# Performance work log

Measured on AMD Instinct MI355X. Metric: run time of the kernel, lower is better.

## Reference

```python
import jax, jax.numpy as jnp
import numpy as np

B, N, D, H = 8, 1024, 768, 12
HD = D // H
SCALE = HD ** -0.5

def setup_inputs() -> dict:
    key = jax.random.key(0)
    k1, k2, k3, k4 = jax.random.split(key, 4)
    x = jax.random.normal(k1, (B, N, D), dtype=jnp.float32)
    weight = jax.random.uniform(k2, (B, N), dtype=jnp.float32)
    W_qkv = jax.random.normal(k3, (D, 3 * D), dtype=jnp.float32) * (D ** -0.5)
    W_msa = jax.random.normal(k4, (D, D), dtype=jnp.float32) * (D ** -0.5)
    b_msa = jnp.zeros((D,), dtype=jnp.float32)
    return {"x": x, "weight": weight, "W_qkv": W_qkv, "W_msa": W_msa, "b_msa": b_msa}

def reference(x, weight, W_qkv, W_msa, b_msa):
    # QKV projection (no bias), then elementwise per-token gate
    qkv = jnp.einsum('bnd,de->bne', x, W_qkv)          # [B,N,3D]
    qkv = weight[:, :, None] * qkv
    qkv = qkv.reshape(B, N, 3, H, HD).transpose(2, 0, 3, 1, 4)  # [3,B,H,N,hd]
    q, k, v = qkv[0], qkv[1], qkv[2]
    A = jnp.einsum('bhnd,bhmd->bhnm', q, k) * SCALE    # [B,H,N,N]
    A = jax.nn.softmax(A, axis=-1)
    out = jnp.einsum('bhnm,bhmd->bhnd', A, v)          # [B,H,N,hd]
    out = out.transpose(0, 2, 1, 3).reshape(B, N, D)
    return jnp.einsum('bnd,de->bne', out, W_msa) + b_msa
```

## Files before the change

### kernel.cpp

```cpp
#include <hip/hip_runtime.h>
#include <hip/hip_bf16.h>


typedef __attribute__((ext_vector_type(8))) short bf8;
typedef __attribute__((ext_vector_type(4))) float f4;

#define QSCALE 0.1803368801111204f
#define MFMA16 __builtin_amdgcn_mfma_f32_16x16x32_bf16

static __device__ __forceinline__ short bf16_of(float f) {
    union { float f; unsigned u; } a; a.f = f;
    unsigned r = a.u + 0x7FFFu + ((a.u >> 16) & 1u);
    return (short)(r >> 16);
}

static __device__ __forceinline__ unsigned bfpk(float lo, float hi) {
    float2 t; t.x = lo; t.y = hi;
    __hip_bfloat162 b = __float22bfloat162_rn(t);
    union { __hip_bfloat162 b; unsigned u; } c; c.b = b;
    return c.u;
}

static __device__ __forceinline__ void async16(const short* g, short* l) {
    __builtin_amdgcn_global_load_lds(
        (const __attribute__((address_space(1))) void*)g,
        (__attribute__((address_space(3))) void*)l, 16, 0, 0);
}

static __device__ __forceinline__ void transpose64(
        const float* __restrict__ w, short* __restrict__ wt,
        int K, int E, int k0, int e0, int tid, short (*t)[65]) {
#pragma unroll
    for (int p = 0; p < 16; ++p) {
        int idx = p * 256 + tid;
        int r = idx >> 6, c = idx & 63;
        t[r][c] = bf16_of(w[(k0 + r) * E + e0 + c]);
    }
    __syncthreads();
#pragma unroll
    for (int p = 0; p < 16; ++p) {
        int idx = p * 256 + tid;
        int r = idx >> 6, c = idx & 63;
        wt[(e0 + r) * K + k0 + c] = t[c][r];
    }
}

__global__ __launch_bounds__(256) void k_prep(
        const float* __restrict__ x, const float* __restrict__ gate,
        short* __restrict__ xb,
        const float* __restrict__ Wqkv, short* __restrict__ wtq,
        const float* __restrict__ Wmsa, short* __restrict__ wtm) {
    __shared__ short t[64][65];
    const int bid = blockIdx.x, tid = threadIdx.x;
    if (bid < 3072) {
        int i = bid * 256 + tid;
        const float g = gate[i / 96];
        const f4* sp = (const f4*)x;
        f4 a = sp[2 * i], b = sp[2 * i + 1];
        union { bf8 v; short h[8]; } o;
        o.h[0] = bf16_of(a[0] * g); o.h[1] = bf16_of(a[1] * g);
        o.h[2] = bf16_of(a[2] * g); o.h[3] = bf16_of(a[3] * g);
        o.h[4] = bf16_of(b[0] * g); o.h[5] = bf16_of(b[1] * g);
        o.h[6] = bf16_of(b[2] * g); o.h[7] = bf16_of(b[7 - 4] * g);
        o.h[6] = bf16_of(b[2] * g); o.h[7] = bf16_of(b[3] * g);
        ((bf8*)xb)[i] = o.v;
    } else if (bid < 3504) {
        int tt = bid - 3072;
        transpose64(Wqkv, wtq, 768, 2304, (tt / 36) * 64, (tt % 36) * 64, tid, t);
    } else {
        int tt = bid - 3504;
        transpose64(Wmsa, wtm, 768, 768, (tt / 12) * 64, (tt % 12) * 64, tid, t);
    }
}

__global__ __launch_bounds__(256, 2) void k_gemm_qkv(
        const short* __restrict__ xb, const short* __restrict__ wtq,
        short* __restrict__ qb, short* __restrict__ kb, short* __restrict__ vt) {
    __shared__ short lds[34816];
    const int tid = threadIdx.x, lane = tid & 63;
    const int l16 = lane & 15, quad = lane >> 4;
    const int wm = tid >> 6;

    const int wg = blockIdx.x;
    const int swz = (wg & 7) * 128 + (wg >> 3);
    const int mI = swz >> 4, nI = swz & 15;
    const int m0 = mI * 128, n0 = nI * 144;

    const short* gA = xb + m0 * 768;
    const short* gB = wtq + n0 * 768;

    auto stage = [&](int buf, int k0) {
        short* base = lds + buf * 8704;
#pragma unroll
        for (int j = 0; j < 2; ++j) {
            int p = j * 256 + tid, row = p >> 2;
            int gc = (p & 3) ^ ((row >> 1) & 3);
            async16(gA + row * 768 + k0 + gc * 8, base + p * 8);
        }
#pragma unroll
        for (int j = 0; j < 2; ++j) {
            int p = j * 256 + tid, row = p >> 2;
            int gc = (p & 3) ^ ((row >> 1) & 3);
            async16(gB + row * 768 + k0 + gc * 8, base + 4096 + p * 8);
        }
        if (tid < 64) {
            int p = 512 + tid, row = p >> 2;
            int gc = (p & 3) ^ ((row >> 1) & 3);
            async16(gB + row * 768 + k0 + gc * 8, base + 4096 + p * 8);
        }
    };

    auto rdA = [&](const short* base, int mf) {
        int row = wm * 32 + mf * 16 + l16;
        return *(const bf8*)(base + row * 32 +
                             ((quad ^ ((row >> 1) & 3)) << 3));
    };
    auto rdB = [&](const short* base, int nf) {
        int row = nf * 16 + l16;
        return *(const bf8*)(base + 4096 + row * 32 +
                             ((quad ^ ((row >> 1) & 3)) << 3));
    };

    f4 z = {0.f, 0.f, 0.f, 0.f};
    f4 acc[2][9];
#pragma unroll
    for (int mf = 0; mf < 2; ++mf)
#pragma unroll
        for (int nf = 0; nf < 9; ++nf) acc[mf][nf] = z;

    stage(0, 0); stage(1, 32); stage(2, 64);
    if (wm == 0) asm volatile("s_waitcnt vmcnt(10)" ::: "memory");
    else         asm volatile("s_waitcnt vmcnt(8)" ::: "memory");
    __builtin_amdgcn_s_barrier();

#pragma unroll 4
    for (int t = 0; t < 24; ++t) {
        const short* cur = lds + (t & 3) * 8704;
        bf8 af0 = rdA(cur, 0);
        bf8 af1 = rdA(cur, 1);
        bf8 bfr[9];
#pragma unroll
        for (int nf = 0; nf < 9; ++nf) bfr[nf] = rdB(cur, nf);
        if (t < 21) stage((t + 3) & 3, (t + 3) * 32);
        __builtin_amdgcn_s_setprio(1);
#pragma unroll
        for (int nf = 0; nf < 9; ++nf) {
            acc[0][nf] = MFMA16(af0, bfr[nf], acc[0][nf], 0, 0, 0);
            acc[1][nf] = MFMA16(af1, bfr[nf], acc[1][nf], 0, 0, 0);
        }
        __builtin_amdgcn_s_setprio(0);
        if (t < 21) {
            if (wm == 0) asm volatile("s_waitcnt vmcnt(10)" ::: "memory");
            else         asm volatile("s_waitcnt vmcnt(8)" ::: "memory");
        } else if (t == 21) {
            if (wm == 0) asm volatile("s_waitcnt vmcnt(5)" ::: "memory");
            else         asm volatile("s_waitcnt vmcnt(4)" ::: "memory");
        } else if (t == 22) {
            asm volatile("s_waitcnt vmcnt(0)" ::: "memory");
        }
        if (t < 23) __builtin_amdgcn_s_barrier();
    }

    const int bI = m0 >> 10, nn0 = m0 & 1023;
#pragma unroll
    for (int nf = 0; nf < 9; ++nf) {
        const int ct = n0 + nf * 16;
        if (ct < 1536) {
            const int which = (ct >= 768) ? 1 : 0;
            const int h = (ct - which * 768) >> 6;
            const int hd = (ct & 63) + l16;
            short* dst = (which ? kb : qb) + (bI * 12 + h) * 65536 + hd;
#pragma unroll
            for (int mf = 0; mf < 2; ++mf)
#pragma unroll
                for (int r = 0; r < 4; ++r) {
                    const int nn = nn0 + wm * 32 + mf * 16 + quad * 4 + r;
                    const float val = acc[mf][nf][r];
                    dst[nn * 64] = bf16_of(which ? val : val * QSCALE);
                }
        }
    }
    const int vlo = (n0 >= 1536) ? n0 : 1536;
    const int vcnt = n0 + 144 - vlo;
    const int npass = (vcnt > 0) ? vcnt / 48 : 0;
    for (int p = 0; p < npass; ++p) {
        __syncthreads();
        const int c0 = vlo + p * 48;
#pragma unroll
        for (int nf = 0; nf < 9; ++nf) {
            const int ct = n0 + nf * 16;
            if (ct >= c0 && ct < c0 + 48) {
                const int lcol = ct - c0 + l16;
#pragma unroll
                for (int mf = 0; mf < 2; ++mf)
#pragma unroll
                    for (int r = 0; r < 4; ++r) {
                        const int row = wm * 32 + mf * 16 + quad * 4 + r;
                        lds[lcol * 136 + row] = bf16_of(acc[mf][nf][r]);
                    }
            }
        }
        __syncthreads();
        const int vg0 = c0 - 1536;
#pragma unroll
        for (int u = 0; u < 3; ++u) {
            const int idx = u * 256 + tid;
            const int lc = idx >> 4, ck = idx & 15;
            const int vg = vg0 + lc;
            const int h = vg >> 6, hd = vg & 63;
            bf8 vv = *(const bf8*)(lds + lc * 136 + ck * 8);
            *(bf8*)(vt + ((bI * 12 + h) * 64 + hd) * 1024 + nn0 + ck * 8) = vv;
        }
    }
}

__global__ __launch_bounds__(256, 2) void k_gemm_final(
        const short* __restrict__ attn, const short* __restrict__ wtm,
        const float* __restrict__ bias, float* __restrict__ out) {
    __shared__ short lds[28672];
    const int tid = threadIdx.x, lane = tid & 63;
    const int l16 = lane & 15, quad = lane >> 4, rx = l16 & 7;
    const int wm = tid >> 6;

    const int wg = blockIdx.x;
    const int swz = (wg & 7) * 64 + (wg >> 3);
    const int mI = swz >> 3, nI = swz & 7;
    const int m0 = mI * 128, n0 = nI * 96;

    const short* gA = attn + m0 * 768;
    const short* gB = wtm + n0 * 768;

    auto stageA = [&](int buf, int k0) {
        short* base = lds + buf * 14336;
#pragma unroll
        for (int j = 0; j < 4; ++j) {
            int p = j * 256 + tid, row = p >> 3;
            int gc = (p & 7) ^ (row & 7);
            async16(gA + row * 768 + k0 + gc * 8, base + p * 8);
        }
    };
    auto stageB = [&](int buf, int k0) {
        short* base = lds + buf * 14336 + 8192;
#pragma unroll
        for (int j = 0; j < 3; ++j) {
            int p = j * 256 + tid, row = p >> 3;
            int gc = (p & 7) ^ (row & 7);
            async16(gB + row * 768 + k0 + gc * 8, base + p * 8);
        }
    };
    auto rdA = [&](const short* base, int mf, int ks) {
        return *(const bf8*)(base + (wm * 32 + mf * 16 + l16) * 64 +
                             (((ks * 4 + quad) ^ rx) << 3));
    };
    auto rdB = [&](const short* base, int nf, int ks) {
        return *(const bf8*)(base + 8192 + (nf * 16 + l16) * 64 +
                             (((ks * 4 + quad) ^ rx) << 3));
    };

    f4 z = {0.f, 0.f, 0.f, 0.f};
    f4 acc[2][6];
#pragma unroll
    for (int mf = 0; mf < 2; ++mf)
#pragma unroll
        for (int nf = 0; nf < 6; ++nf) acc[mf][nf] = z;

    stageA(0, 0); stageB(0, 0);
    asm volatile("s_waitcnt vmcnt(0)" ::: "memory");
    __builtin_amdgcn_s_barrier();

#pragma unroll 2
    for (int t = 0; t < 12; ++t) {
        const short* cur = lds + (t & 1) * 14336;
        bf8 af[2][2];
        af[0][0] = rdA(cur, 0, 0); af[0][1] = rdA(cur, 0, 1);
        af[1][0] = rdA(cur, 1, 0); af[1][1] = rdA(cur, 1, 1);
        bf8 bfr[3][2];
#pragma unroll
        for (int nf = 0; nf < 3; ++nf) { bfr[nf][0] = rdB(cur, nf, 0); bfr[nf][1] = rdB(cur, nf, 1); }
        if (t < 11) stageA((t + 1) & 1, (t + 1) * 64);
        __builtin_amdgcn_s_setprio(1);
#pragma unroll
        for (int mf = 0; mf < 2; ++mf)
#pragma unroll
            for (int nf = 0; nf < 3; ++nf) {
                acc[mf][nf] = MFMA16(af[mf][0], bfr[nf][0], acc[mf][nf], 0, 0, 0);
                acc[mf][nf] = MFMA16(af[mf][1], bfr[nf][1], acc[mf][nf], 0, 0, 0);
            }
        __builtin_amdgcn_s_setprio(0);
        bf8 bfh[3][2];
#pragma unroll
        for (int nf = 0; nf < 3; ++nf) { bfh[nf][0] = rdB(cur, nf + 3, 0); bfh[nf][1] = rdB(cur, nf + 3, 1); }
        if (t < 11) stageB((t + 1) & 1, (t + 1) * 64);
        __builtin_amdgcn_s_setprio(1);
#pragma unroll
        for (int mf = 0; mf < 2; ++mf)
#pragma unroll
            for (int nf = 0; nf < 3; ++nf) {
                acc[mf][nf + 3] = MFMA16(af[mf][0], bfh[nf][0], acc[mf][nf + 3], 0, 0, 0);
                acc[mf][nf + 3] = MFMA16(af[mf][1], bfh[nf][1], acc[mf][nf + 3], 0, 0, 0);
            }
        __builtin_amdgcn_s_setprio(0);
        asm volatile("s_waitcnt vmcnt(0)" ::: "memory");
        __builtin_amdgcn_s_barrier();
    }

#pragma unroll
    for (int nf = 0; nf < 6; ++nf) {
        const int e = n0 + nf * 16 + l16;
        const float bv = bias[e];
#pragma unroll
        for (int mf = 0; mf < 2; ++mf)
#pragma unroll
            for (int r = 0; r < 4; ++r) {
                const int row = m0 + wm * 32 + mf * 16 + quad * 4 + r;
                out[row * 768 + e] = acc[mf][nf][r] + bv;
            }
    }
}

__global__ __launch_bounds__(256, 3) void k_attn(const short* __restrict__ qb,
                                                 const short* __restrict__ kb,
                                                 const short* __restrict__ vt,
                                                 short* __restrict__ attn) {
    __shared__ short Ks[2][4096];
    __shared__ short Vs[2][4096];
    const int tid = threadIdx.x, wave = tid >> 6, lane = tid & 63;
    const int l16 = lane & 15, quad = lane >> 4;
    const int bh = blockIdx.x;
    const int b = bh / 12, h = bh - b * 12;
    const int m_base = blockIdx.y * 128 + wave * 32;
    const short* qh = qb + bh * 65536;
    const short* kh = kb + bh * 65536;
    const short* vh = vt + bh * 65536;

    const int rA = ((l16 >> 2) << 3) + (l16 & 3);
    const int fK = (((rA >> 3) & 1) << 2) + (rA & 3);
    const int sK = (quad ^ fK) * 8;
    const int oAlo = rA * 64 + sK;
    const int oAhi = rA * 64 + (sK ^ 32);
    const int oBlo = oAlo + 256, oBhi = oAhi + 256;
    const int fV = (((l16 >> 3) & 1) << 2) + (l16 & 3);
    const int oV = l16 * 64 + ((quad ^ fV) * 8);

    const short* qp0 = qh + (m_base + l16) * 64 + quad * 8;
    bf8 qf00 = *(const bf8*)(qp0);
    bf8 qf01 = *(const bf8*)(qp0 + 32);
    const short* qp1 = qp0 + 16 * 64;
    bf8 qf10 = *(const bf8*)(qp1);
    bf8 qf11 = *(const bf8*)(qp1 + 32);

    union { bf8 v; short h[8]; } onef;
#pragma unroll
    for (int i = 0; i < 8; ++i) onef.h[i] = (short)0x3F80;

    f4 z = {0.f, 0.f, 0.f, 0.f};
    f4 acc0[4] = {z, z, z, z};
    f4 acc1[4] = {z, z, z, z};
    f4 accl0 = z, accl1 = z;

    auto stage = [&](int buf, int j0) {
#pragma unroll
        for (int j = 0; j < 2; ++j) {
            int idx = j * 256 + tid;
            int row = idx >> 3;
            int fr = (((row >> 3) & 1) << 2) + (row & 3);
            int gc = (idx & 7) ^ fr;
            async16(kh + (j0 + row) * 64 + gc * 8, Ks[buf] + idx * 8);
            async16(vh + row * 1024 + j0 + gc * 8, Vs[buf] + idx * 8);
        }
    };

    stage(0, 0);
    int cur = 0;
    for (int it = 0; it < 16; ++it) {
        __builtin_amdgcn_s_waitcnt(0);
        __syncthreads();
        if (it + 1 < 16) stage(cur ^ 1, (it + 1) * 64);
        const short* Kc = Ks[cur];
        const short* Vc = Vs[cur];

#pragma unroll
        for (int jj = 0; jj < 64; jj += 32) {
            const short* kjj = Kc + jj * 64;
            bf8 kAlo = *(const bf8*)(kjj + oAlo);
            bf8 kAhi = *(const bf8*)(kjj + oAhi);
            bf8 kBlo = *(const bf8*)(kjj + oBlo);
            bf8 kBhi = *(const bf8*)(kjj + oBhi);
            bf8 vf0 = *(const bf8*)(Vc + 0 * 1024 + (oV ^ (jj ? 32 : 0)));
            bf8 vf1 = *(const bf8*)(Vc + 1 * 1024 + (oV ^ (jj ? 32 : 0)));
            bf8 vf2 = *(const bf8*)(Vc + 2 * 1024 + (oV ^ (jj ? 32 : 0)));
            bf8 vf3 = *(const bf8*)(Vc + 3 * 1024 + (oV ^ (jj ? 32 : 0)));

            {
                f4 sA = z, sB = z;
                __builtin_amdgcn_s_setprio(1);
                sA = MFMA16(kAlo, qf00, sA, 0, 0, 0);
                sA = MFMA16(kAhi, qf01, sA, 0, 0, 0);
                sB = MFMA16(kBlo, qf00, sB, 0, 0, 0);
                sB = MFMA16(kBhi, qf01, sB, 0, 0, 0);
                __builtin_amdgcn_s_setprio(0);
                float a0 = __builtin_amdgcn_exp2f(sA[0]);
                float a1 = __builtin_amdgcn_exp2f(sA[1]);
                float a2 = __builtin_amdgcn_exp2f(sA[2]);
                float a3 = __builtin_amdgcn_exp2f(sA[3]);
                float b0 = __builtin_amdgcn_exp2f(sB[0]);
                float b1 = __builtin_amdgcn_exp2f(sB[1]);
                float b2 = __builtin_amdgcn_exp2f(sB[2]);
                float b3 = __builtin_amdgcn_exp2f(sB[3]);
                union { bf8 v; unsigned u[4]; } p;
                p.u[0] = bfpk(a0, a1); p.u[1] = bfpk(a2, a3);
                p.u[2] = bfpk(b0, b1); p.u[3] = bfpk(b2, b3);
                __builtin_amdgcn_s_setprio(1);
                accl0 = MFMA16(onef.v, p.v, accl0, 0, 0, 0);
                acc0[0] = MFMA16(vf0, p.v, acc0[0], 0, 0, 0);
                acc0[1] = MFMA16(vf1, p.v, acc0[1], 0, 0, 0);
                acc0[2] = MFMA16(vf2, p.v, acc0[2], 0, 0, 0);
                acc0[3] = MFMA16(vf3, p.v, acc0[3], 0, 0, 0);
                __builtin_amdgcn_s_setprio(0);
            }
            {
                f4 sA = z, sB = z;
                __builtin_amdgcn_s_setprio(1);
                sA = MFMA16(kAlo, qf10, sA, 0, 0, 0);
                sA = MFMA16(kAhi, qf11, sA, 0, 0, 0);
                sB = MFMA16(kBlo, qf10, sB, 0, 0, 0);
                sB = MFMA16(kBhi, qf11, sB, 0, 0, 0);
                __builtin_amdgcn_s_setprio(0);
                float a0 = __builtin_amdgcn_exp2f(sA[0]);
                float a1 = __builtin_amdgcn_exp2f(sA[1]);
                float a2 = __builtin_amdgcn_exp2f(sA[2]);
                float a3 = __builtin_amdgcn_exp2f(sA[3]);
                float b0 = __builtin_amdgcn_exp2f(sB[0]);
                float b1 = __builtin_amdgcn_exp2f(sB[1]);
                float b2 = __builtin_amdgcn_exp2f(sB[2]);
                float b3 = __builtin_amdgcn_exp2f(sB[3]);
                union { bf8 v; unsigned u[4]; } p;
                p.u[0] = bfpk(a0, a1); p.u[1] = bfpk(a2, a3);
                p.u[2] = bfpk(b0, b1); p.u[3] = bfpk(b2, b3);
                __builtin_amdgcn_s_setprio(1);
                accl1 = MFMA16(onef.v, p.v, accl1, 0, 0, 0);
                acc1[0] = MFMA16(vf0, p.v, acc1[0], 0, 0, 0);
                acc1[1] = MFMA16(vf1, p.v, acc1[1], 0, 0, 0);
                acc1[2] = MFMA16(vf2, p.v, acc1[2], 0, 0, 0);
                acc1[3] = MFMA16(vf3, p.v, acc1[3], 0, 0, 0);
                __builtin_amdgcn_s_setprio(0);
            }
        }
        cur ^= 1;
    }

    const float inv0 = 1.f / accl0[0];
    const float inv1 = 1.f / accl1[0];
    const int row0 = (b << 10) + m_base + l16;
    short* op0 = attn + row0 * 768 + h * 64 + quad * 4;
    short* op1 = op0 + 16 * 768;
#pragma unroll
    for (int dt = 0; dt < 4; ++dt)
#pragma unroll
        for (int r = 0; r < 4; ++r) {
            op0[dt * 16 + r] = bf16_of(acc0[dt][r] * inv0);
            op1[dt * 16 + r] = bf16_of(acc1[dt][r] * inv1);
        }
}

extern "C" void kernel_launch(void* const* d_in, const int* in_sizes, int n_in,
                              void* d_out, int out_size, void* d_ws, size_t ws_size,
                              hipStream_t stream) {
    const float* x    = (const float*)d_in[0];
    const float* gate = (const float*)d_in[1];
    const float* Wqkv = (const float*)d_in[2];
    const float* Wmsa = (const float*)d_in[3];
    const float* bmsa = (const float*)d_in[4];
    float* out = (float*)d_out;

    char* ws = (char*)d_ws;
    short* xb  = (short*)(ws);
    short* wtq = (short*)(ws + 12582912);
    short* wtm = (short*)(ws + 16121856);
    short* qb  = (short*)(ws + 17301504);
    short* kb  = (short*)(ws + 29884416);
    short* vt  = (short*)(ws + 42467328);
    short* attn = xb;

    k_prep<<<3648, 256, 0, stream>>>(x, gate, xb, Wqkv, wtq, Wmsa, wtm);
    k_gemm_qkv<<<1024, 256, 0, stream>>>(xb, wtq, qb, kb, vt);
    k_attn<<<dim3(96, 8), 256, 0, stream>>>(qb, kb, vt, attn);
    k_gemm_final<<<512, 256, 0, stream>>>(attn, wtm, bmsa, out);
}
```

Baseline: 172.0 us.

## Enlarge QKV GEMM tile to 128x288 with 2x2 wave grid and triple buffering

The QKV projection GEMM now uses 128x288 output tiles per workgroup, split across a 2x2 wave layout with each wave computing 64x144. The grid halves to 512 workgroups, and the LDS pipeline goes from four stages to three to fit the larger tiles. The aim is more MFMA work per LDS fragment load and less redundant A-tile loading from global memory. The cost is many more accumulator registers (36 f4 per wave), fewer workgroups in the grid, and a shallower prefetch depth.

```diff
diff --git a/kernel.cpp b/kernel.cpp
--- a/kernel.cpp
+++ b/kernel.cpp
@@ -61,7 +61,6 @@
         o.h[0] = bf16_of(a[0] * g); o.h[1] = bf16_of(a[1] * g);
         o.h[2] = bf16_of(a[2] * g); o.h[3] = bf16_of(a[3] * g);
         o.h[4] = bf16_of(b[0] * g); o.h[5] = bf16_of(b[1] * g);
-        o.h[6] = bf16_of(b[2] * g); o.h[7] = bf16_of(b[7 - 4] * g);
         o.h[6] = bf16_of(b[2] * g); o.h[7] = bf16_of(b[3] * g);
         ((bf8*)xb)[i] = o.v;
     } else if (bid < 3504) {
@@ -76,21 +75,21 @@
 __global__ __launch_bounds__(256, 2) void k_gemm_qkv(
         const short* __restrict__ xb, const short* __restrict__ wtq,
         short* __restrict__ qb, short* __restrict__ kb, short* __restrict__ vt) {
-    __shared__ short lds[34816];
+    __shared__ short lds[39936];
     const int tid = threadIdx.x, lane = tid & 63;
     const int l16 = lane & 15, quad = lane >> 4;
-    const int wm = tid >> 6;
+    const int wv = tid >> 6, wm = wv >> 1, wn = wv & 1;
 
     const int wg = blockIdx.x;
-    const int swz = (wg & 7) * 128 + (wg >> 3);
-    const int mI = swz >> 4, nI = swz & 15;
-    const int m0 = mI * 128, n0 = nI * 144;
+    const int swz = (wg & 7) * 64 + (wg >> 3);
+    const int mI = swz >> 3, nI = swz & 7;
+    const int m0 = mI * 128, n0 = nI * 288;
 
     const short* gA = xb + m0 * 768;
     const short* gB = wtq + n0 * 768;
 
     auto stage = [&](int buf, int k0) {
-        short* base = lds + buf * 8704;
+        short* base = lds + buf * 13312;
 #pragma unroll
         for (int j = 0; j < 2; ++j) {
             int p = j * 256 + tid, row = p >> 2;
@@ -98,63 +97,61 @@
             async16(gA + row * 768 + k0 + gc * 8, base + p * 8);
         }
 #pragma unroll
-        for (int j = 0; j < 2; ++j) {
+        for (int j = 0; j < 4; ++j) {
             int p = j * 256 + tid, row = p >> 2;
             int gc = (p & 3) ^ ((row >> 1) & 3);
             async16(gB + row * 768 + k0 + gc * 8, base + 4096 + p * 8);
         }
-        if (tid < 64) {
-            int p = 512 + tid, row = p >> 2;
+        if (tid < 128) {
+            int p = 1024 + tid, row = p >> 2;
             int gc = (p & 3) ^ ((row >> 1) & 3);
             async16(gB + row * 768 + k0 + gc * 8, base + 4096 + p * 8);
         }
     };
 
     auto rdA = [&](const short* base, int mf) {
-        int row = wm * 32 + mf * 16 + l16;
+        int row = wm * 64 + mf * 16 + l16;
         return *(const bf8*)(base + row * 32 +
                              ((quad ^ ((row >> 1) & 3)) << 3));
     };
     auto rdB = [&](const short* base, int nf) {
-        int row = nf * 16 + l16;
+        int row = wn * 144 + nf * 16 + l16;
         return *(const bf8*)(base + 4096 + row * 32 +
                              ((quad ^ ((row >> 1) & 3)) << 3));
     };
 
     f4 z = {0.f, 0.f, 0.f, 0.f};
-    f4 acc[2][9];
-#pragma unroll
-    for (int mf = 0; mf < 2; ++mf)
+    f4 acc[4][9];
+#pragma unroll
+    for (int mf = 0; mf < 4; ++mf)
 #pragma unroll
         for (int nf = 0; nf < 9; ++nf) acc[mf][nf] = z;
 
-    stage(0, 0); stage(1, 32); stage(2, 64);
-    if (wm == 0) asm volatile("s_waitcnt vmcnt(10)" ::: "memory");
-    else         asm volatile("s_waitcnt vmcnt(8)" ::: "memory");
+    stage(0, 0); stage(1, 32);
+    if (wv < 2) asm volatile("s_waitcnt vmcnt(7)" ::: "memory");
+    else        asm volatile("s_waitcnt vmcnt(6)" ::: "memory");
     __builtin_amdgcn_s_barrier();
 
-#pragma unroll 4
+#pragma unroll 3
     for (int t = 0; t < 24; ++t) {
-        const short* cur = lds + (t & 3) * 8704;
-        bf8 af0 = rdA(cur, 0);
-        bf8 af1 = rdA(cur, 1);
+        const short* cur = lds + (t % 3) * 13312;
+        bf8 af[4];
+#pragma unroll
+        for (int mf = 0; mf < 4; ++mf) af[mf] = rdA(cur, mf);
         bf8 bfr[9];
 #pragma unroll
         for (int nf = 0; nf < 9; ++nf) bfr[nf] = rdB(cur, nf);
-        if (t < 21) stage((t + 3) & 3, (t + 3) * 32);
+        if (t < 22) stage((t + 2) % 3, (t + 2) * 32);
         __builtin_amdgcn_s_setprio(1);
 #pragma unroll
-        for (int nf = 0; nf < 9; ++nf) {
-            acc[0][nf] = MFMA16(af0, bfr[nf], acc[0][nf], 0, 0, 0);
-            acc[1][nf] = MFMA16(af1, bfr[nf], acc[1][nf], 0, 0, 0);
-        }
+        for (int mf = 0; mf < 4; ++mf)
+#pragma unroll
+            for (int nf = 0; nf < 9; ++nf)
+                acc[mf][nf] = MFMA16(af[mf], bfr[nf], acc[mf][nf], 0, 0, 0);
         __builtin_amdgcn_s_setprio(0);
-        if (t < 21) {
-            if (wm == 0) asm volatile("s_waitcnt vmcnt(10)" ::: "memory");
-            else         asm volatile("s_waitcnt vmcnt(8)" ::: "memory");
-        } else if (t == 21) {
-            if (wm == 0) asm volatile("s_waitcnt vmcnt(5)" ::: "memory");
-            else         asm volatile("s_waitcnt vmcnt(4)" ::: "memory");
+        if (t < 22) {
+            if (wv < 2) asm volatile("s_waitcnt vmcnt(7)" ::: "memory");
+            else        asm volatile("s_waitcnt vmcnt(6)" ::: "memory");
         } else if (t == 22) {
             asm volatile("s_waitcnt vmcnt(0)" ::: "memory");
         }
@@ -164,46 +161,45 @@
     const int bI = m0 >> 10, nn0 = m0 & 1023;
 #pragma unroll
     for (int nf = 0; nf < 9; ++nf) {
-        const int ct = n0 + nf * 16;
+        const int ct = n0 + wn * 144 + nf * 16;
         if (ct < 1536) {
             const int which = (ct >= 768) ? 1 : 0;
             const int h = (ct - which * 768) >> 6;
             const int hd = (ct & 63) + l16;
             short* dst = (which ? kb : qb) + (bI * 12 + h) * 65536 + hd;
 #pragma unroll
-            for (int mf = 0; mf < 2; ++mf)
+            for (int mf = 0; mf < 4; ++mf)
 #pragma unroll
                 for (int r = 0; r < 4; ++r) {
-                    const int nn = nn0 + wm * 32 + mf * 16 + quad * 4 + r;
+                    const int nn = nn0 + wm * 64 + mf * 16 + quad * 4 + r;
                     const float val = acc[mf][nf][r];
                     dst[nn * 64] = bf16_of(which ? val : val * QSCALE);
                 }
         }
     }
-    const int vlo = (n0 >= 1536) ? n0 : 1536;
-    const int vcnt = n0 + 144 - vlo;
-    const int npass = (vcnt > 0) ? vcnt / 48 : 0;
+    const int vstart = (n0 >= 1536) ? n0 : 1536;
+    const int npass = (n0 + 288 > vstart) ? (n0 + 288 - vstart) / 96 : 0;
     for (int p = 0; p < npass; ++p) {
         __syncthreads();
-        const int c0 = vlo + p * 48;
+        const int c0 = vstart + p * 96;
 #pragma unroll
         for (int nf = 0; nf < 9; ++nf) {
-            const int ct = n0 + nf * 16;
-            if (ct >= c0 && ct < c0 + 48) {
-                const int lcol = ct - c0 + l16;
-#pragma unroll
-                for (int mf = 0; mf < 2; ++mf)
+            const int ct = n0 + wn * 144 + nf * 16;
+            if (ct >= c0 && ct < c0 + 96) {
+                const int lc = ct - c0 + l16;
+#pragma unroll
+                for (int mf = 0; mf < 4; ++mf)
 #pragma unroll
                     for (int r = 0; r < 4; ++r) {
-                        const int row = wm * 32 + mf * 16 + quad * 4 + r;
-                        lds[lcol * 136 + row] = bf16_of(acc[mf][nf][r]);
+                        const int row = wm * 64 + mf * 16 + quad * 4 + r;
+                        lds[lc * 136 + row] = bf16_of(acc[mf][nf][r]);
                     }
             }
         }
         __syncthreads();
         const int vg0 = c0 - 1536;
 #pragma unroll
-        for (int u = 0; u < 3; ++u) {
+        for (int u = 0; u < 6; ++u) {
             const int idx = u * 256 + tid;
             const int lc = idx >> 4, ck = idx & 15;
             const int vg = vg0 + lc;
@@ -483,7 +479,7 @@
     short* attn = xb;
 
     k_prep<<<3648, 256, 0, stream>>>(x, gate, xb, Wqkv, wtq, Wmsa, wtm);
-    k_gemm_qkv<<<1024, 256, 0, stream>>>(xb, wtq, qb, kb, vt);
+    k_gemm_qkv<<<512, 256, 0, stream>>>(xb, wtq, qb, kb, vt);
     k_attn<<<dim3(96, 8), 256, 0, stream>>>(qb, kb, vt, attn);
     k_gemm_final<<<512, 256, 0, stream>>>(attn, wtm, bmsa, out);
 }
```

Result: slower. 218.3 us (+26.9%).

## Deepen async LDS pipelines in final GEMM and attention kernels

Applied to the files above, without the earlier changes.

The output-projection GEMM now uses a K-step of 32 with a 4-stage ring of LDS buffers and prefetches three stages ahead. Partial vmcnt waits replace full drains, with different counts per thread group because only half the threads issue the extra B load. The attention kernel moves from double to triple buffering of K/V tiles with vmcnt(4) waits, so global loads stay in flight across iterations. A duplicated store line in the prep kernel is also removed. This adds LDS use and per-thread waitcnt bookkeeping that must exactly match the number of issued loads.

```diff
diff --git a/kernel.cpp b/kernel.cpp
--- a/kernel.cpp
+++ b/kernel.cpp
@@ -61,7 +61,6 @@
         o.h[0] = bf16_of(a[0] * g); o.h[1] = bf16_of(a[1] * g);
         o.h[2] = bf16_of(a[2] * g); o.h[3] = bf16_of(a[3] * g);
         o.h[4] = bf16_of(b[0] * g); o.h[5] = bf16_of(b[1] * g);
-        o.h[6] = bf16_of(b[2] * g); o.h[7] = bf16_of(b[7 - 4] * g);
         o.h[6] = bf16_of(b[2] * g); o.h[7] = bf16_of(b[3] * g);
         ((bf8*)xb)[i] = o.v;
     } else if (bid < 3504) {
@@ -219,7 +218,7 @@
         const float* __restrict__ bias, float* __restrict__ out) {
     __shared__ short lds[28672];
     const int tid = threadIdx.x, lane = tid & 63;
-    const int l16 = lane & 15, quad = lane >> 4, rx = l16 & 7;
+    const int l16 = lane & 15, quad = lane >> 4;
     const int wm = tid >> 6;
 
     const int wg = blockIdx.x;
@@ -230,31 +229,35 @@
     const short* gA = attn + m0 * 768;
     const short* gB = wtm + n0 * 768;
 
-    auto stageA = [&](int buf, int k0) {
-        short* base = lds + buf * 14336;
-#pragma unroll
-        for (int j = 0; j < 4; ++j) {
-            int p = j * 256 + tid, row = p >> 3;
-            int gc = (p & 7) ^ (row & 7);
+    auto stage = [&](int buf, int k0) {
+        short* base = lds + buf * 7168;
+#pragma unroll
+        for (int j = 0; j < 2; ++j) {
+            int p = j * 256 + tid, row = p >> 2;
+            int gc = (p & 3) ^ ((row >> 1) & 3);
             async16(gA + row * 768 + k0 + gc * 8, base + p * 8);
         }
-    };
-    auto stageB = [&](int buf, int k0) {
-        short* base = lds + buf * 14336 + 8192;
-#pragma unroll
-        for (int j = 0; j < 3; ++j) {
-            int p = j * 256 + tid, row = p >> 3;
-            int gc = (p & 7) ^ (row & 7);
-            async16(gB + row * 768 + k0 + gc * 8, base + p * 8);
-        }
-    };
-    auto rdA = [&](const short* base, int mf, int ks) {
-        return *(const bf8*)(base + (wm * 32 + mf * 16 + l16) * 64 +
-                             (((ks * 4 + quad) ^ rx) << 3));
-    };
-    auto rdB = [&](const short* base, int nf, int ks) {
-        return *(const bf8*)(base + 8192 + (nf * 16 + l16) * 64 +
-                             (((ks * 4 + quad) ^ rx) << 3));
+        {
+            int p = tid, row = p >> 2;
+            int gc = (p & 3) ^ ((row >> 1) & 3);
+            async16(gB + row * 768 + k0 + gc * 8, base + 4096 + p * 8);
+        }
+        if (tid < 128) {
+            int p = 256 + tid, row = p >> 2;
+            int gc = (p & 3) ^ ((row >> 1) & 3);
+            async16(gB + row * 768 + k0 + gc * 8, base + 4096 + p * 8);
+        }
+    };
+
+    auto rdA = [&](const short* base, int mf) {
+        int row = wm * 32 + mf * 16 + l16;
+        return *(const bf8*)(base + row * 32 +
+                             ((quad ^ ((row >> 1) & 3)) << 3));
+    };
+    auto rdB = [&](const short* base, int nf) {
+        int row = nf * 16 + l16;
+        return *(const bf8*)(base + 4096 + row * 32 +
+                             ((quad ^ ((row >> 1) & 3)) << 3));
     };
 
     f4 z = {0.f, 0.f, 0.f, 0.f};
@@ -264,44 +267,37 @@
 #pragma unroll
         for (int nf = 0; nf < 6; ++nf) acc[mf][nf] = z;
 
-    stageA(0, 0); stageB(0, 0);
-    asm volatile("s_waitcnt vmcnt(0)" ::: "memory");
+    stage(0, 0); stage(1, 32); stage(2, 64);
+    if (tid < 128) asm volatile("s_waitcnt vmcnt(8)" ::: "memory");
+    else           asm volatile("s_waitcnt vmcnt(6)" ::: "memory");
     __builtin_amdgcn_s_barrier();
 
-#pragma unroll 2
-    for (int t = 0; t < 12; ++t) {
-        const short* cur = lds + (t & 1) * 14336;
-        bf8 af[2][2];
-        af[0][0] = rdA(cur, 0, 0); af[0][1] = rdA(cur, 0, 1);
-        af[1][0] = rdA(cur, 1, 0); af[1][1] = rdA(cur, 1, 1);
-        bf8 bfr[3][2];
-#pragma unroll
-        for (int nf = 0; nf < 3; ++nf) { bfr[nf][0] = rdB(cur, nf, 0); bfr[nf][1] = rdB(cur, nf, 1); }
-        if (t < 11) stageA((t + 1) & 1, (t + 1) * 64);
+#pragma unroll 4
+    for (int t = 0; t < 24; ++t) {
+        const short* cur = lds + (t & 3) * 7168;
+        bf8 af0 = rdA(cur, 0);
+        bf8 af1 = rdA(cur, 1);
+        bf8 bfr[6];
+#pragma unroll
+        for (int nf = 0; nf < 6; ++nf) bfr[nf] = rdB(cur, nf);
+        if (t < 21) stage((t + 3) & 3, (t + 3) * 32);
         __builtin_amdgcn_s_setprio(1);
 #pragma unroll
-        for (int mf = 0; mf < 2; ++mf)
-#pragma unroll
-            for (int nf = 0; nf < 3; ++nf) {
-                acc[mf][nf] = MFMA16(af[mf][0], bfr[nf][0], acc[mf][nf], 0, 0, 0);
-                acc[mf][nf] = MFMA16(af[mf][1], bfr[nf][1], acc[mf][nf], 0, 0, 0);
-            }
+        for (int nf = 0; nf < 6; ++nf) {
+            acc[0][nf] = MFMA16(af0, bfr[nf], acc[0][nf], 0, 0, 0);
+            acc[1][nf] = MFMA16(af1, bfr[nf], acc[1][nf], 0, 0, 0);
+        }
         __builtin_amdgcn_s_setprio(0);
-        bf8 bfh[3][2];
-#pragma unroll
-        for (int nf = 0; nf < 3; ++nf) { bfh[nf][0] = rdB(cur, nf + 3, 0); bfh[nf][1] = rdB(cur, nf + 3, 1); }
-        if (t < 11) stageB((t + 1) & 1, (t + 1) * 64);
-        __builtin_amdgcn_s_setprio(1);
-#pragma unroll
-        for (int mf = 0; mf < 2; ++mf)
-#pragma unroll
-            for (int nf = 0; nf < 3; ++nf) {
-                acc[mf][nf + 3] = MFMA16(af[mf][0], bfh[nf][0], acc[mf][nf + 3], 0, 0, 0);
-                acc[mf][nf + 3] = MFMA16(af[mf][1], bfh[nf][1], acc[mf][nf + 3], 0, 0, 0);
-            }
-        __builtin_amdgcn_s_setprio(0);
-        asm volatile("s_waitcnt vmcnt(0)" ::: "memory");
-        __builtin_amdgcn_s_barrier();
+        if (t < 21) {
+            if (tid < 128) asm volatile("s_waitcnt vmcnt(8)" ::: "memory");
+            else           asm volatile("s_waitcnt vmcnt(6)" ::: "memory");
+        } else if (t == 21) {
+            if (tid < 128) asm volatile("s_waitcnt vmcnt(4)" ::: "memory");
+            else           asm volatile("s_waitcnt vmcnt(3)" ::: "memory");
+        } else if (t == 22) {
+            asm volatile("s_waitcnt vmcnt(0)" ::: "memory");
+        }
+        if (t < 23) __builtin_amdgcn_s_barrier();
     }
 
 #pragma unroll
@@ -322,8 +318,8 @@
                                                  const short* __restrict__ kb,
                                                  const short* __restrict__ vt,
                                                  short* __restrict__ attn) {
-    __shared__ short Ks[2][4096];
-    __shared__ short Vs[2][4096];
+    __shared__ short Ks[3][4096];
+    __shared__ short Vs[3][4096];
     const int tid = threadIdx.x, wave = tid >> 6, lane = tid & 63;
     const int l16 = lane & 15, quad = lane >> 4;
     const int bh = blockIdx.x;
@@ -370,14 +366,14 @@
         }
     };
 
-    stage(0, 0);
-    int cur = 0;
+    stage(0, 0); stage(1, 64);
     for (int it = 0; it < 16; ++it) {
-        __builtin_amdgcn_s_waitcnt(0);
-        __syncthreads();
-        if (it + 1 < 16) stage(cur ^ 1, (it + 1) * 64);
-        const short* Kc = Ks[cur];
-        const short* Vc = Vs[cur];
+        if (it < 15) asm volatile("s_waitcnt vmcnt(4)" ::: "memory");
+        else         asm volatile("s_waitcnt vmcnt(0)" ::: "memory");
+        __builtin_amdgcn_s_barrier();
+        if (it + 2 < 16) stage((it + 2) % 3, (it + 2) * 64);
+        const short* Kc = Ks[it % 3];
+        const short* Vc = Vs[it % 3];
 
 #pragma unroll
         for (int jj = 0; jj < 64; jj += 32) {
@@ -446,7 +442,6 @@
                 __builtin_amdgcn_s_setprio(0);
             }
         }
-        cur ^= 1;
     }
 
     const float inv0 = 1.f / accl0[0];
```

Result: no change. 175.0 us (+1.7%).
